# Performance work log

Measured on AMD Instinct MI355X. Metric: run time of the kernel, lower is better.

## Reference

```python
import jax, jax.numpy as jnp
import numpy as np

E = 8      # num_experts
D = 512    # input feature dim
H1 = 512   # expert_hidden[0]
H2 = 256   # expert_hidden[1]
Y = 256    # y_dim
B = 8192   # batch
ALPHA = 0.2


def setup_inputs() -> dict:
    key = jax.random.key(0)
    ks = jax.random.split(key, 8)
    h = jax.random.normal(ks[0], (B, D), dtype=jnp.float32)
    gate_id = jax.random.randint(ks[1], (B,), 0, E, dtype=jnp.int64)
    # Per-expert MLP parameters, stacked over expert axis (Glorot-ish scale)
    W1 = jax.random.normal(ks[2], (E, D, H1), dtype=jnp.float32) * (1.0 / np.sqrt(D))
    b1 = jnp.zeros((E, H1), dtype=jnp.float32)
    W2 = jax.random.normal(ks[3], (E, H1, H2), dtype=jnp.float32) * (1.0 / np.sqrt(H1))
    b2 = jnp.zeros((E, H2), dtype=jnp.float32)
    W3 = jax.random.normal(ks[4], (E, H2, Y), dtype=jnp.float32) * (1.0 / np.sqrt(H2))
    b3 = jnp.zeros((E, Y), dtype=jnp.float32)
    return {"h": h, "gate_id": gate_id, "W1": W1, "b1": b1,
            "W2": W2, "b2": b2, "W3": W3, "b3": b3}


def _leaky(x):
    return jnp.where(x > 0, x, ALPHA * x)


def reference(h, gate_id, W1, b1, W2, b2, W3, b3):
    # Hard routing: gate_id = clip(round(gate_id), 0, E-1)
    g = jnp.clip(jnp.round(gate_id.astype(jnp.float32)).astype(jnp.int32), 0, E - 1)
    # Dense all-experts compute (jit-friendly, no dynamic shapes), then select
    # the routed expert's output per row. Same math as dispatch/stitch.
    a1 = _leaky(jnp.einsum('bd,edh->ebh', h, W1) + b1[:, None, :])   # [E,B,H1]
    a2 = _leaky(jnp.einsum('ebh,ehk->ebk', a1, W2) + b2[:, None, :]) # [E,B,H2]
    y = jnp.einsum('ebk,eky->eby', a2, W3) + b3[:, None, :]          # [E,B,Y]
    out = y[g, jnp.arange(h.shape[0])]                                # [B,Y]
    return out
```

## Files before the change

kernel.cpp:

```cpp
#include <hip/hip_runtime.h>
#include <stdint.h>

#define NE 8
#define ND 512
#define NH1 512
#define NH2 256
#define NY 256
#define NB 8192
#define BM3 32
#define MAXT3 (NB/BM3 + NE - 1)
#define W1T64 (NE * (ND/64) * (NH1/64))
#define W2T64 (NE * (NH1/64) * (NH2/64))
#define W3T64 (NE * (NH2/64) * (NY/64))
#define WTT64 (W1T64 + W2T64 + W3T64)

typedef float f32x4 __attribute__((ext_vector_type(4)));
typedef __bf16 bf16x8 __attribute__((ext_vector_type(8)));
typedef unsigned short u16x8 __attribute__((ext_vector_type(8)));

__device__ __forceinline__ unsigned short f2bf(float f) {
  unsigned int u = __float_as_uint(f);
  u += 0x7fffu + ((u >> 16) & 1u);
  return (unsigned short)(u >> 16);
}

__device__ __forceinline__ int clampe(int g) {
  return g < 0 ? 0 : (g > NE - 1 ? NE - 1 : g);
}



__global__ __launch_bounds__(256)
void prep_k(const int* __restrict__ gate,
            const float* __restrict__ W1, const float* __restrict__ W2,
            const float* __restrict__ W3,
            unsigned short* __restrict__ w1f, unsigned short* __restrict__ w2f,
            unsigned short* __restrict__ w3f,
            int* __restrict__ meta, int* __restrict__ perm)
{
  __shared__ char sm[17024] __attribute__((aligned(16)));
  int b = blockIdx.x, t = threadIdx.x;

  if (b < WTT64) {
    float* ldsf = (float*)sm;
    const float* src; unsigned short* dst; int K, N, idx;
    if (b < W1T64)          { src = W1; dst = w1f; K = ND;  N = NH1; idx = b; }
    else if (b < W1T64 + W2T64) { src = W2; dst = w2f; K = NH1; N = NH2; idx = b - W1T64; }
    else                    { src = W3; dst = w3f; K = NH2; N = NY;  idx = b - W1T64 - W2T64; }
    int ntn = N >> 6, ntk = K >> 6;
    int n0 = (idx % ntn) * 64;
    int k0 = ((idx / ntn) % ntk) * 64;
    int g  = idx / (ntn * ntk);

    {
      int r  = t >> 2;
      int c4 = t & 3;
      const float* s = src + (size_t)g * K * N + (size_t)(k0 + r) * N + n0;
      #pragma unroll
      for (int i = 0; i < 4; i++) {
        float4 v = *(const float4*)(s + (i * 4 + c4) * 4);
        *(float4*)(ldsf + r * 65 + (i * 4 + c4) * 4) = v;
      }
    }
    __syncthreads();

    unsigned short* d = dst + (size_t)g * K * N;
    #pragma unroll
    for (int ii = 0; ii < 2; ii++) {
      int idx2 = ii * 256 + t;
      int lane = idx2 & 63;
      int f    = (idx2 >> 6) & 3;
      int kt   = idx2 >> 8;
      int kl   = kt * 32 + (lane >> 4) * 8;
      int nl   = f * 16 + (lane & 15);
      union { u16x8 v; unsigned short u[8]; } pk;
      #pragma unroll
      for (int j = 0; j < 8; j++)
        pk.u[j] = f2bf(ldsf[(kl + j) * 65 + nl]);
      int ktg = (k0 >> 5) + kt;
      int fg  = (n0 >> 4) + f;
      *(u16x8*)(d + (((size_t)ktg * (N >> 4) + fg) * 64 + lane) * 8) = pk.v;
    }
    return;
  }

  unsigned int* lcnt_lo = (unsigned int*)sm;
  unsigned int* lcnt_hi = lcnt_lo + 256;
  int* pre   = (int*)(sm + 2048);
  int* cnt8  = (int*)(sm + 2048 + 8192);
  int* offs8 = cnt8 + 8;

  unsigned int gp[8];
  unsigned int clo = 0, chi = 0;
  #pragma unroll
  for (int i = 0; i < 32; i++) {
    int g = clampe(gate[t * 32 + i]);
    if ((i & 3) == 0) gp[i >> 2] = 0;
    gp[i >> 2] |= (unsigned int)g << (8 * (i & 3));
    if (g < 4) clo += 1u << (8 * g);
    else       chi += 1u << (8 * (g - 4));
  }
  lcnt_lo[t] = clo;
  lcnt_hi[t] = chi;
  __syncthreads();

  int wave = t >> 6, lane = t & 63;
  #pragma unroll
  for (int pass = 0; pass < 2; pass++) {
    int e = wave + pass * 4;
    int carry = 0;
    #pragma unroll
    for (int ch = 0; ch < 4; ch++) {
      int idx = ch * 64 + lane;
      unsigned int word = (e < 4) ? lcnt_lo[idx] : lcnt_hi[idx];
      int v = (int)((word >> (8 * (e & 3))) & 255u);
      int s = v;
      #pragma unroll
      for (int d = 1; d < 64; d <<= 1) {
        int up = __shfl_up(s, d, 64);
        if (lane >= d) s += up;
      }
      pre[e * 256 + idx] = carry + s - v;
      carry += __shfl(s, 63, 64);
    }
    if (lane == 0) cnt8[e] = carry;
  }
  __syncthreads();

  if (t == 0) {
    int off = 0, tt2 = 0;
    for (int e = 0; e < NE; e++) {
      int cc = cnt8[e];
      meta[e] = cc;
      meta[8 + e] = off;
      offs8[e] = off;
      int ntl = (cc + BM3 - 1) / BM3;
      for (int i = 0; i < ntl; i++) meta[1024 + tt2++] = (e << 16) | i;
      off += cc;
    }
    meta[24] = tt2;
  }
  __syncthreads();

  unsigned int rlo = 0, rhi = 0;
  #pragma unroll
  for (int i = 0; i < 32; i++) {
    int g = (int)((gp[i >> 2] >> (8 * (i & 3))) & 255u);
    int r;
    if (g < 4) { r = (int)((rlo >> (8 * g)) & 255u);       rlo += 1u << (8 * g); }
    else       { r = (int)((rhi >> (8 * (g - 4))) & 255u); rhi += 1u << (8 * (g - 4)); }
    perm[offs8[g] + pre[g * 256 + t] + r] = t * 32 + i;
  }
}

__global__ __launch_bounds__(512, 6)
void mlp_k(const float* __restrict__ h,
           const float* __restrict__ b1, const float* __restrict__ b2,
           const float* __restrict__ b3,
           float* __restrict__ out,
           const int* __restrict__ meta, const int* __restrict__ perm,
           const unsigned short* __restrict__ w1f,
           const unsigned short* __restrict__ w2f,
           const unsigned short* __restrict__ w3f)
{
  __shared__ unsigned short sA[BM3 * 520];
  __shared__ unsigned short sB[BM3 * 520];
  __shared__ int permc[BM3];

  if ((int)blockIdx.x >= meta[24]) return;

  int tid  = threadIdx.x;
  int ent  = meta[1024 + blockIdx.x];
  int e    = ent >> 16;
  int trow = ent & 0xffff;
  int cnt  = meta[e];
  int off  = meta[8 + e];
  int row0 = trow * BM3;

  if (tid < BM3) {
    int grow = row0 + tid;
    permc[tid] = (grow < cnt) ? perm[off + grow] : 0;
  }
  __syncthreads();

  int wave = tid >> 6, lane = tid & 63;
  int lm = lane & 15, quad = lane >> 4;

  {
    int r  = tid >> 4;
    int cb = (tid & 15) * 8;
    const float* hrow = h + (size_t)permc[r] * ND;
    #pragma unroll
    for (int jj = 0; jj < 4; jj++) {
      int col = cb + jj * 128;
      float4 f0 = *(const float4*)(hrow + col);
      float4 f1 = *(const float4*)(hrow + col + 4);
      union { u16x8 v; unsigned short u[8]; } pk;
      pk.u[0] = f2bf(f0.x); pk.u[1] = f2bf(f0.y); pk.u[2] = f2bf(f0.z); pk.u[3] = f2bf(f0.w);
      pk.u[4] = f2bf(f1.x); pk.u[5] = f2bf(f1.y); pk.u[6] = f2bf(f1.z); pk.u[7] = f2bf(f1.w);
      *(u16x8*)(sA + r * 520 + col) = pk.v;
    }
  }
  __syncthreads();

  f32x4 zero = {0.f, 0.f, 0.f, 0.f};

  {
    f32x4 acc[2][4];
    #pragma unroll
    for (int mi = 0; mi < 2; mi++)
      #pragma unroll
      for (int ni = 0; ni < 4; ni++)
        acc[mi][ni] = zero;
    const unsigned short* Wb = w1f + (size_t)e * ND * NH1 + ((size_t)(wave * 4) * 64 + lane) * 8;
    bf16x8 cur[4], nxt[4];
    #pragma unroll
    for (int ni = 0; ni < 4; ni++)
      cur[ni] = *reinterpret_cast<const bf16x8*>(Wb + ni * 512);
    for (int t = 0; t < 16; t++) {
      int tn = (t + 1 < 16) ? t + 1 : t;
      #pragma unroll
      for (int ni = 0; ni < 4; ni++)
        nxt[ni] = *reinterpret_cast<const bf16x8*>(Wb + (size_t)tn * 16384 + ni * 512);
      bf16x8 af[2];
      #pragma unroll
      for (int mi = 0; mi < 2; mi++)
        af[mi] = *reinterpret_cast<const bf16x8*>(sA + (mi * 16 + lm) * 520 + t * 32 + quad * 8);
      #pragma unroll
      for (int mi = 0; mi < 2; mi++)
        #pragma unroll
        for (int ni = 0; ni < 4; ni++)
          acc[mi][ni] = __builtin_amdgcn_mfma_f32_16x16x32_bf16(af[mi], cur[ni], acc[mi][ni], 0, 0, 0);
      #pragma unroll
      for (int ni = 0; ni < 4; ni++)
        cur[ni] = nxt[ni];
    }
    #pragma unroll
    for (int mi = 0; mi < 2; mi++)
      #pragma unroll
      for (int ni = 0; ni < 4; ni++) {
        int col = (wave * 4 + ni) * 16 + lm;
        float bv = b1[e * NH1 + col];
        #pragma unroll
        for (int r = 0; r < 4; r++) {
          int row = mi * 16 + quad * 4 + r;
          float v = acc[mi][ni][r] + bv;
          v = (v > 0.f) ? v : 0.2f * v;
          sB[row * 520 + col] = f2bf(v);
        }
      }
  }
  __syncthreads();

  {
    f32x4 acc[2][2];
    #pragma unroll
    for (int mi = 0; mi < 2; mi++)
      #pragma unroll
      for (int ni = 0; ni < 2; ni++)
        acc[mi][ni] = zero;
    const unsigned short* Wb = w2f + (size_t)e * NH1 * NH2 + ((size_t)(wave * 2) * 64 + lane) * 8;
    bf16x8 cur[2], nxt[2];
    #pragma unroll
    for (int ni = 0; ni < 2; ni++)
      cur[ni] = *reinterpret_cast<const bf16x8*>(Wb + ni * 512);
    for (int t = 0; t < 16; t++) {
      int tn = (t + 1 < 16) ? t + 1 : t;
      #pragma unroll
      for (int ni = 0; ni < 2; ni++)
        nxt[ni] = *reinterpret_cast<const bf16x8*>(Wb + (size_t)tn * 8192 + ni * 512);
      bf16x8 af[2];
      #pragma unroll
      for (int mi = 0; mi < 2; mi++)
        af[mi] = *reinterpret_cast<const bf16x8*>(sB + (mi * 16 + lm) * 520 + t * 32 + quad * 8);
      #pragma unroll
      for (int mi = 0; mi < 2; mi++)
        #pragma unroll
        for (int ni = 0; ni < 2; ni++)
          acc[mi][ni] = __builtin_amdgcn_mfma_f32_16x16x32_bf16(af[mi], cur[ni], acc[mi][ni], 0, 0, 0);
      #pragma unroll
      for (int ni = 0; ni < 2; ni++)
        cur[ni] = nxt[ni];
    }
    #pragma unroll
    for (int mi = 0; mi < 2; mi++)
      #pragma unroll
      for (int ni = 0; ni < 2; ni++) {
        int col = (wave * 2 + ni) * 16 + lm;
        float bv = b2[e * NH2 + col];
        #pragma unroll
        for (int r = 0; r < 4; r++) {
          int row = mi * 16 + quad * 4 + r;
          float v = acc[mi][ni][r] + bv;
          v = (v > 0.f) ? v : 0.2f * v;
          sA[row * 264 + col] = f2bf(v);
        }
      }
  }
  __syncthreads();

  {
    f32x4 acc[2][2];
    #pragma unroll
    for (int mi = 0; mi < 2; mi++)
      #pragma unroll
      for (int ni = 0; ni < 2; ni++)
        acc[mi][ni] = zero;
    const unsigned short* Wb = w3f + (size_t)e * NH2 * NY + ((size_t)(wave * 2) * 64 + lane) * 8;
    bf16x8 cur[2], nxt[2];
    #pragma unroll
    for (int ni = 0; ni < 2; ni++)
      cur[ni] = *reinterpret_cast<const bf16x8*>(Wb + ni * 512);
    for (int t = 0; t < 8; t++) {
      int tn = (t + 1 < 8) ? t + 1 : t;
      #pragma unroll
      for (int ni = 0; ni < 2; ni++)
        nxt[ni] = *reinterpret_cast<const bf16x8*>(Wb + (size_t)tn * 8192 + ni * 512);
      bf16x8 af[2];
      #pragma unroll
      for (int mi = 0; mi < 2; mi++)
        af[mi] = *reinterpret_cast<const bf16x8*>(sA + (mi * 16 + lm) * 264 + t * 32 + quad * 8);
      #pragma unroll
      for (int mi = 0; mi < 2; mi++)
        #pragma unroll
        for (int ni = 0; ni < 2; ni++)
          acc[mi][ni] = __builtin_amdgcn_mfma_f32_16x16x32_bf16(af[mi], cur[ni], acc[mi][ni], 0, 0, 0);
      #pragma unroll
      for (int ni = 0; ni < 2; ni++)
        cur[ni] = nxt[ni];
    }
    #pragma unroll
    for (int mi = 0; mi < 2; mi++)
      #pragma unroll
      for (int ni = 0; ni < 2; ni++) {
        int col = (wave * 2 + ni) * 16 + lm;
        float bv = b3[e * NY + col];
        #pragma unroll
        for (int r = 0; r < 4; r++) {
          int row = mi * 16 + quad * 4 + r;
          int grow = row0 + row;
          if (grow < cnt) {
            float v = acc[mi][ni][r] + bv;
            __builtin_nontemporal_store(v, &out[(size_t)permc[row] * NY + col]);
          }
        }
      }
  }
}

extern "C" void kernel_launch(void* const* d_in, const int* in_sizes, int n_in,
                              void* d_out, int out_size, void* d_ws, size_t ws_size,
                              hipStream_t stream) {
  (void)in_sizes; (void)n_in; (void)out_size; (void)ws_size;
  const float* h  = (const float*)d_in[0];
  const int* gate = (const int*)d_in[1];
  const float* W1 = (const float*)d_in[2];
  const float* b1 = (const float*)d_in[3];
  const float* W2 = (const float*)d_in[4];
  const float* b2 = (const float*)d_in[5];
  const float* W3 = (const float*)d_in[6];
  const float* b3 = (const float*)d_in[7];
  float* out = (float*)d_out;

  char* ws = (char*)d_ws;
  int* meta = (int*)ws;
  int* perm = (int*)(ws + 8192);
  unsigned short* w1f = (unsigned short*)(ws + 8192 + 32768);
  unsigned short* w2f = w1f + (size_t)NE * ND * NH1;
  unsigned short* w3f = w2f + (size_t)NE * NH1 * NH2;

  prep_k<<<WTT64 + 1, 256, 0, stream>>>(gate, W1, W2, W3, w1f, w2f, w3f, meta, perm);
  mlp_k<<<MAXT3, 512, 0, stream>>>(h, b1, b2, b3, out, meta, perm, w1f, w2f, w3f);
}
```

Baseline: 118.5 us.

## Claim expert tiles dynamically by XCC id to improve L2 weight locality

Replaces the static tile list with dynamic tile claiming. Each block reads its XCC id from a hardware register, then takes tiles through an atomic counter, trying its matching expert first and moving to other experts afterward. The goal is to keep each expert's bf16 weights resident in one XCC's L2 instead of spreading them across all XCCs. This adds a global atomic per block and fixes the grid at 320 blocks, so tiles beyond that count would be left unprocessed.

Measured after the change: 116.9 us. Within noise of the previous version (-1.3%).

```diff
diff --git a/kernel.cpp b/kernel.cpp
--- a/kernel.cpp
+++ b/kernel.cpp
@@ -8,7 +8,7 @@
 #define NY 256
 #define NB 8192
 #define BM3 32
-#define MAXT3 (NB/BM3 + NE - 1)
+#define NBPE 40
 #define W1T64 (NE * (ND/64) * (NH1/64))
 #define W2T64 (NE * (NH1/64) * (NH2/64))
 #define W3T64 (NE * (NH2/64) * (NY/64))
@@ -128,17 +128,16 @@
   __syncthreads();
 
   if (t == 0) {
-    int off = 0, tt2 = 0;
+    int off = 0;
     for (int e = 0; e < NE; e++) {
       int cc = cnt8[e];
       meta[e] = cc;
       meta[8 + e] = off;
       offs8[e] = off;
-      int ntl = (cc + BM3 - 1) / BM3;
-      for (int i = 0; i < ntl; i++) meta[1024 + tt2++] = (e << 16) | i;
+      meta[16 + e] = (cc + BM3 - 1) / BM3;
+      meta[32 + e] = 0;
       off += cc;
     }
-    meta[24] = tt2;
   }
   __syncthreads();
 
@@ -158,7 +157,7 @@
            const float* __restrict__ b1, const float* __restrict__ b2,
            const float* __restrict__ b3,
            float* __restrict__ out,
-           const int* __restrict__ meta, const int* __restrict__ perm,
+           int* __restrict__ meta, const int* __restrict__ perm,
            const unsigned short* __restrict__ w1f,
            const unsigned short* __restrict__ w2f,
            const unsigned short* __restrict__ w3f)
@@ -166,13 +165,27 @@
   __shared__ unsigned short sA[BM3 * 520];
   __shared__ unsigned short sB[BM3 * 520];
   __shared__ int permc[BM3];
-
-  if ((int)blockIdx.x >= meta[24]) return;
+  __shared__ int sclaim[2];
 
   int tid  = threadIdx.x;
-  int ent  = meta[1024 + blockIdx.x];
-  int e    = ent >> 16;
-  int trow = ent & 0xffff;
+
+  if (tid == 0) {
+    int xcc = (int)__builtin_amdgcn_s_getreg((31 << 11) | 20) & (NE - 1);
+    int ce = -1, cti = 0;
+    for (int a = 0; a < NE; a++) {
+      int ee = (xcc + a) & (NE - 1);
+      int ntl = meta[16 + ee];
+      if (ntl <= 0) continue;
+      int tk = atomicAdd(&meta[32 + ee], 1);
+      if (tk < ntl) { ce = ee; cti = tk; break; }
+    }
+    sclaim[0] = ce; sclaim[1] = cti;
+  }
+  __syncthreads();
+
+  int e = sclaim[0];
+  if (e < 0) return;
+  int trow = sclaim[1];
   int cnt  = meta[e];
   int off  = meta[8 + e];
   int row0 = trow * BM3;
@@ -370,5 +383,5 @@
   unsigned short* w3f = w2f + (size_t)NE * NH1 * NH2;
 
   prep_k<<<WTT64 + 1, 256, 0, stream>>>(gate, W1, W2, W3, w1f, w2f, w3f, meta, perm);
-  mlp_k<<<MAXT3, 512, 0, stream>>>(h, b1, b2, b3, out, meta, perm, w1f, w2f, w3f);
-}
+  mlp_k<<<NE * NBPE, 512, 0, stream>>>(h, b1, b2, b3, out, meta, perm, w1f, w2f, w3f);
+}
```
